# Performance work log

Hardware: AMD Instinct MI355X
Metric: run time of the kernel (lower is better)

## Reference

```python
import jax, jax.numpy as jnp
import numpy as np

N, R, M, E, NE, B = 50000, 500, 120000, 960000, 800000, 8192
D, H1, HID, OC = 200, 256, 512, 50


def setup_inputs() -> dict:
    key = jax.random.key(0)
    ks = jax.random.split(key, 26)
    s = 0.05
    rn = lambda k, shp: jax.random.normal(k, shp, jnp.float32) * s
    return {
        "entity_emb": jax.random.normal(ks[0], (N, D), jnp.float32),
        "rel_emb": jax.random.normal(ks[1], (R, D), jnp.float32),
        "b_x": jax.random.randint(ks[2], (M,), 0, N),
        "b_node_graph_index": jax.random.randint(ks[3], (M,), 0, R),
        "edge_src": jax.random.randint(ks[4], (E,), 0, M),
        "edge_dst": jax.random.randint(ks[5], (E,), 0, M),
        "edge_w": jax.random.uniform(ks[6], (E,), jnp.float32),
        "big_src": jax.random.randint(ks[7], (NE,), 0, N),
        "big_dst": jax.random.randint(ks[8], (NE,), 0, N),
        "big_w": jax.random.uniform(ks[9], (NE,), jnp.float32),
        "perm": jax.random.permutation(ks[10], N),
        "batch_inputs": jnp.stack([
            jax.random.randint(ks[11], (B,), 0, N),
            jax.random.randint(ks[12], (B,), 0, R),
            jax.random.randint(ks[13], (B,), 0, N)], axis=1),
        "W1a": rn(ks[14], (2 * D, H1)), "W1b": rn(ks[15], (H1, D)),
        "W2a": rn(ks[16], (D, H1)), "W2b": rn(ks[17], (H1, D)),
        "Wle": rn(ks[18], (2 * D, 1)), "ble": jnp.zeros((1,), jnp.float32),
        "Wlo": rn(ks[19], (2 * D, D)), "blo": jnp.zeros((D,), jnp.float32),
        "Wg": rn(ks[20], (D, HID)), "Wd": rn(ks[21], (HID, HID)),
        "conv_w": rn(ks[22], (OC, 3)), "conv_b": jnp.zeros((OC,), jnp.float32),
        "fc_w": rn(ks[23], (OC * D, 1)), "fc_b": jnp.zeros((1,), jnp.float32),
    }


def _l2norm(x):
    return x / jnp.maximum(jnp.linalg.norm(x, axis=-1, keepdims=True), 1e-12)


def _gcn(x, src, dst, w, n, Wa, Wb):
    # two-layer GCN over sparse edge list: out = A @ relu(A @ x @ Wa) @ Wb
    agg = lambda h: jax.ops.segment_sum(h[src] * w[:, None], dst, num_segments=n)
    h = jax.nn.relu(agg(x) @ Wa)
    return agg(h) @ Wb


def _seg_softmax(v, idx, n):
    m = jax.ops.segment_max(v, idx, num_segments=n)
    e = jnp.exp(v - m[idx])
    s = jax.ops.segment_sum(e, idx, num_segments=n)
    return e / (s[idx] + 1e-16)


def _mce(ent, rel, b_x, b_gi, src, dst, w, W1a, W1b, Wle, ble, Wlo, blo):
    x = jnp.concatenate([ent[b_x], rel[b_gi]], axis=-1)          # [M, 400]
    e = _gcn(x, src, dst, w, b_x.shape[0], W1a, W1b)             # [M, 200]
    cnt = jax.ops.segment_sum(jnp.ones((b_x.shape[0],), e.dtype), b_x, num_segments=N)
    mean = jax.ops.segment_sum(e, b_x, num_segments=N) / jnp.maximum(cnt, 1.0)[:, None]
    z = mean[b_x]                                                # scatter_mean then gather
    emb = jnp.concatenate([e[b_x], z], axis=-1)                  # [M, 400]
    score = emb @ Wle + ble                                      # [M, 1]
    zs = _seg_softmax(score, b_x, N)                             # segment softmax
    pooled = jax.ops.segment_sum(zs * emb, b_x, num_segments=N)  # [N, 400]
    return (pooled @ Wlo + blo) + ent


def _dgi(h1, h2, Wg, Wd):
    p1 = jax.nn.relu(h1 @ Wg)
    p2 = jax.nn.relu(h2 @ Wg)
    c = jax.nn.sigmoid(jnp.mean(p1, axis=0))                     # readout [HID]
    t = Wd @ c
    return jnp.concatenate([p1 @ t, p2 @ t])                     # [2N]


def _convkb(trip, conv_w, conv_b, fc_w, fc_b):
    # trip [B,3,D]; Conv2d(1, OC, (1,3)) over [B,1,D,3] -> [B,OC,D]
    h = jax.nn.relu(jnp.einsum('bsd,os->bod', trip, conv_w) + conv_b[None, :, None])
    return h.reshape(trip.shape[0], -1) @ fc_w + fc_b            # [B,1]


def reference(entity_emb, rel_emb, b_x, b_node_graph_index, edge_src, edge_dst,
              edge_w, big_src, big_dst, big_w, perm, batch_inputs,
              W1a, W1b, W2a, W2b, Wle, ble, Wlo, blo, Wg, Wd,
              conv_w, conv_b, fc_w, fc_b):
    ent = _l2norm(entity_emb)
    rel = _l2norm(rel_emb)
    ent_shuf = ent[perm]
    ec = _mce(ent, rel, b_x, b_node_graph_index, edge_src, edge_dst, edge_w,
              W1a, W1b, Wle, ble, Wlo, blo)
    ec_ = _mce(ent_shuf, rel, b_x, b_node_graph_index, edge_src, edge_dst, edge_w,
               W1a, W1b, Wle, ble, Wlo, blo)
    eg = _gcn(ec, big_src, big_dst, big_w, N, W2a, W2b)
    eg_ = _gcn(ec_, big_src, big_dst, big_w, N, W2a, W2b)
    local_logits = _dgi(ec, ec_, Wg, Wd)
    global_logits = _dgi(eg, eg_, Wg, Wd)
    trip = jnp.stack([ec[batch_inputs[:, 0]], rel[batch_inputs[:, 1]],
                      ec[batch_inputs[:, 2]]], axis=1)           # [B,3,D]
    out_conv = _convkb(trip, conv_w, conv_b, fc_w, fc_b)
    return out_conv, local_logits, global_logits
```

## Files before the change

kernel.cpp:

```cpp
#include <hip/hip_runtime.h>

#define NN   50000
#define RR   500
#define MM   120000
#define EE   960000
#define NEE  800000
#define BB   8192
#define DD   200
#define HH1  256
#define HIDD 512
#define OCC  50

typedef unsigned int  u32;
typedef unsigned short u16;
typedef __attribute__((ext_vector_type(8))) short bf16x8;
typedef __attribute__((ext_vector_type(4))) float f32x4;

static __device__ __forceinline__ float bf2f(u16 u) {
    u32 x = ((u32)u) << 16;
    return __uint_as_float(x);
}
static __device__ __forceinline__ u16 f2bf(float f) {
    u32 x = __float_as_uint(f);
    u32 r = (x + 0x7FFFu + ((x >> 16) & 1u)) >> 16;
    return (u16)r;
}
static __device__ __forceinline__ u32 pack2(float a, float b) {
    return (u32)f2bf(a) | ((u32)f2bf(b) << 16);
}
static __device__ __forceinline__ void unpack2(u32 v, float& a, float& b) {
    a = bf2f((u16)(v & 0xFFFFu));
    b = bf2f((u16)(v >> 16));
}

static __device__ __forceinline__ float wredsum(float v) {
#pragma unroll
    for (int off = 32; off > 0; off >>= 1) v += __shfl_xor(v, off);
    return v;
}

static __device__ __forceinline__ u32 relu2bf(u32 x) {
    if (x & 0x00008000u) x &= 0xFFFF0000u;
    if (x & 0x80000000u) x &= 0x0000FFFFu;
    return x;
}
static __device__ __forceinline__ bf16x8 zero8() {
    bf16x8 z;
#pragma unroll
    for (int i = 0; i < 8; ++i) z[i] = 0;
    return z;
}

__global__ void k_l2norm(const float* __restrict__ in, float* __restrict__ outf,
                         u16* __restrict__ outb, int rows) {
    int w = (blockIdx.x * blockDim.x + threadIdx.x) >> 6;
    int lane = threadIdx.x & 63;
    if (w >= rows) return;
    const float* r = in + (size_t)w * DD;
    float s = 0.f;
    for (int d = lane; d < DD; d += 64) { float v = r[d]; s += v * v; }
    s = wredsum(s);
    float inv = 1.0f / fmaxf(sqrtf(s), 1e-12f);
    for (int d = lane; d < DD; d += 64) {
        float v = r[d] * inv;
        if (outf) outf[(size_t)w * DD + d] = v;
        if (outb) outb[(size_t)w * DD + d] = f2bf(v);
    }
}

__global__ void k_gather_perm(const int* __restrict__ bx, const int* __restrict__ perm,
                              int* __restrict__ idx1, int M) {
    int m = blockIdx.x * blockDim.x + threadIdx.x;
    if (m < M) idx1[m] = perm[bx[m]];
}

__global__ void k_edge_idx(const int* __restrict__ srcE, const int* __restrict__ map,
                           int* __restrict__ outE, int n) {
    int e = blockIdx.x * blockDim.x + threadIdx.x;
    if (e < n) outE[e] = map[srcE[e]];
}

__global__ void k_prepw(const float* __restrict__ src, int Nc, int Kd,
                        u16* __restrict__ hi, u16* __restrict__ lo) {
    int i = blockIdx.x * blockDim.x + threadIdx.x;
    if (i >= Nc * Kd) return;
    int n = i / Kd, k = i - n * Kd;
    float b = src[(size_t)k * Nc + n];
    u16 hb_ = f2bf(b);
    hi[i] = hb_;
    lo[i] = f2bf(b - bf2f(hb_));
}

__global__ void k_hist(const int* __restrict__ idx, int* __restrict__ cnt, int n) {
    int i = blockIdx.x * blockDim.x + threadIdx.x;
    if (i < n) atomicAdd(&cnt[idx[i]], 1);
}

__global__ __launch_bounds__(1024) void k_scan(const int* __restrict__ in,
                                               int* __restrict__ out, int n) {
    __shared__ int wtot[16];
    __shared__ int wexc[16];
    __shared__ int s_carry;
    int tid = threadIdx.x, lane = tid & 63, wid = tid >> 6;
    if (tid == 0) s_carry = 0;
    __syncthreads();
    for (int base = 0; base < n; base += 1024) {
        int i = base + tid;
        int v = (i < n) ? in[i] : 0;
        int x = v;
#pragma unroll
        for (int off = 1; off < 64; off <<= 1) {
            int t = __shfl_up(x, off);
            if (lane >= off) x += t;
        }
        if (lane == 63) wtot[wid] = x;
        __syncthreads();
        if (wid == 0) {
            int wv2 = (lane < 16) ? wtot[lane] : 0;
            int y = wv2;
#pragma unroll
            for (int off = 1; off < 16; off <<= 1) {
                int t = __shfl_up(y, off);
                if (lane >= off) y += t;
            }
            if (lane < 16) wexc[lane] = y - wv2;
            if (lane == 15) wtot[15] = y;
        }
        __syncthreads();
        if (i < n) out[i] = s_carry + wexc[wid] + (x - v);
        int chunk_total = wtot[15];
        __syncthreads();
        if (tid == 0) s_carry += chunk_total;
        __syncthreads();
    }
    if (threadIdx.x == 0) out[n] = s_carry;
}

__global__ void k_fill2(const int* __restrict__ dst, const int* __restrict__ src,
                        const float* __restrict__ w, int* __restrict__ cursor,
                        int* __restrict__ srcs_out, float* __restrict__ ws_out, int n) {
    int e = blockIdx.x * blockDim.x + threadIdx.x;
    if (e >= n) return;
    int p = atomicAdd(&cursor[dst[e]], 1);
    srcs_out[p] = src[e];
    ws_out[p] = w[e];
}

__global__ void k_fill1(const int* __restrict__ idx, int* __restrict__ cursor,
                        int* __restrict__ outm, int n) {
    int m = blockIdx.x * blockDim.x + threadIdx.x;
    if (m >= n) return;
    int p = atomicAdd(&cursor[idx[m]], 1);
    outm[p] = m;
}

__global__ void k_pull_mce(const int* __restrict__ rp, const int* __restrict__ ivE,
                           const int* __restrict__ giE, const float* __restrict__ wE,
                           const u16* __restrict__ Pent, const u16* __restrict__ Prel,
                           u16* __restrict__ out, int ndst) {
    int wv = (blockIdx.x * blockDim.x + threadIdx.x) >> 6;
    if (wv >= ndst) return;
    int lane = threadIdx.x & 63;
    int beg = rp[wv], end = rp[wv + 1];
    float accA[2] = {0.f, 0.f}, accB[2] = {0.f, 0.f};
    int e = beg;
    for (; e + 4 <= end; e += 4) {
        int i0 = ivE[e], i1 = ivE[e + 1], i2 = ivE[e + 2], i3 = ivE[e + 3];
        int g0 = giE[e], g1 = giE[e + 1], g2 = giE[e + 2], g3 = giE[e + 3];
        float w0 = wE[e], w1 = wE[e + 1], w2 = wE[e + 2], w3 = wE[e + 3];
        const u32* pe0 = (const u32*)(Pent + (size_t)i0 * HH1);
        const u32* pe1 = (const u32*)(Pent + (size_t)i1 * HH1);
        const u32* pe2 = (const u32*)(Pent + (size_t)i2 * HH1);
        const u32* pe3 = (const u32*)(Pent + (size_t)i3 * HH1);
        const u32* pr0 = (const u32*)(Prel + (size_t)g0 * HH1);
        const u32* pr1 = (const u32*)(Prel + (size_t)g1 * HH1);
        const u32* pr2 = (const u32*)(Prel + (size_t)g2 * HH1);
        const u32* pr3 = (const u32*)(Prel + (size_t)g3 * HH1);
        u32 vp[4][2], vr[4][2];
#pragma unroll
        for (int t = 0; t < 2; ++t) {
            int p = lane + 64 * t;
            vp[0][t] = pe0[p]; vp[1][t] = pe1[p]; vp[2][t] = pe2[p]; vp[3][t] = pe3[p];
            vr[0][t] = pr0[p]; vr[1][t] = pr1[p]; vr[2][t] = pr2[p]; vr[3][t] = pr3[p];
        }
#pragma unroll
        for (int t = 0; t < 2; ++t) {
            float a, b, c, d;
            unpack2(vp[0][t], a, b); unpack2(vr[0][t], c, d);
            accA[t] += (a + c) * w0; accB[t] += (b + d) * w0;
            unpack2(vp[1][t], a, b); unpack2(vr[1][t], c, d);
            accA[t] += (a + c) * w1; accB[t] += (b + d) * w1;
            unpack2(vp[2][t], a, b); unpack2(vr[2][t], c, d);
            accA[t] += (a + c) * w2; accB[t] += (b + d) * w2;
            unpack2(vp[3][t], a, b); unpack2(vr[3][t], c, d);
            accA[t] += (a + c) * w3; accB[t] += (b + d) * w3;
        }
    }
    for (; e < end; ++e) {
        int iv = ivE[e], gi = giE[e];
        float w = wE[e];
        const u32* pe = (const u32*)(Pent + (size_t)iv * HH1);
        const u32* pr = (const u32*)(Prel + (size_t)gi * HH1);
#pragma unroll
        for (int t = 0; t < 2; ++t) {
            int p = lane + 64 * t;
            float a, b, c, d;
            unpack2(pe[p], a, b); unpack2(pr[p], c, d);
            accA[t] += (a + c) * w; accB[t] += (b + d) * w;
        }
    }
    u32* o = (u32*)(out + (size_t)wv * HH1);
#pragma unroll
    for (int t = 0; t < 2; ++t) o[lane + 64 * t] = pack2(accA[t], accB[t]);
}

template<int DIMS, int INS, int OUTS>
__global__ void k_pull(const int* __restrict__ rp, const int* __restrict__ srcs,
                       const float* __restrict__ wsrt,
                       const u16* __restrict__ inh, const u16* __restrict__ inl,
                       u16* __restrict__ outh, u16* __restrict__ outl, int ndst) {
    int wv = (blockIdx.x * blockDim.x + threadIdx.x) >> 6;
    if (wv >= ndst) return;
    int lane = threadIdx.x & 63;
    int beg = rp[wv], end = rp[wv + 1];
    constexpr int NP = DIMS / 2;
    constexpr int NT = (NP + 63) / 64;
    float accA[NT], accB[NT];
#pragma unroll
    for (int t = 0; t < NT; ++t) { accA[t] = 0.f; accB[t] = 0.f; }
    int e = beg;
    for (; e + 4 <= end; e += 4) {
        int s0 = srcs[e], s1 = srcs[e + 1], s2 = srcs[e + 2], s3 = srcs[e + 3];
        float w0 = wsrt[e], w1 = wsrt[e + 1], w2 = wsrt[e + 2], w3 = wsrt[e + 3];
        const u32* rh[4] = {
            (const u32*)(inh + (size_t)s0 * DIMS), (const u32*)(inh + (size_t)s1 * DIMS),
            (const u32*)(inh + (size_t)s2 * DIMS), (const u32*)(inh + (size_t)s3 * DIMS)};
        u32 vh[4][NT], vl[4][NT];
#pragma unroll
        for (int t = 0; t < NT; ++t) {
            int p = lane + 64 * t;
            if (p < NP) {
                vh[0][t] = rh[0][p]; vh[1][t] = rh[1][p];
                vh[2][t] = rh[2][p]; vh[3][t] = rh[3][p];
            }
        }
        if (INS) {
            const u32* rl[4] = {
                (const u32*)(inl + (size_t)s0 * DIMS), (const u32*)(inl + (size_t)s1 * DIMS),
                (const u32*)(inl + (size_t)s2 * DIMS), (const u32*)(inl + (size_t)s3 * DIMS)};
#pragma unroll
            for (int t = 0; t < NT; ++t) {
                int p = lane + 64 * t;
                if (p < NP) {
                    vl[0][t] = rl[0][p]; vl[1][t] = rl[1][p];
                    vl[2][t] = rl[2][p]; vl[3][t] = rl[3][p];
                }
            }
        }
        float ws[4] = {w0, w1, w2, w3};
#pragma unroll
        for (int q = 0; q < 4; ++q) {
#pragma unroll
            for (int t = 0; t < NT; ++t) {
                int p = lane + 64 * t;
                if (p < NP) {
                    float a, b;
                    unpack2(vh[q][t], a, b);
                    if (INS) { float a2, b2; unpack2(vl[q][t], a2, b2); a += a2; b += b2; }
                    accA[t] += a * ws[q]; accB[t] += b * ws[q];
                }
            }
        }
    }
    for (; e < end; ++e) {
        int s = srcs[e];
        float w = wsrt[e];
        const u32* rh = (const u32*)(inh + (size_t)s * DIMS);
        const u32* rl = INS ? (const u32*)(inl + (size_t)s * DIMS) : nullptr;
#pragma unroll
        for (int t = 0; t < NT; ++t) {
            int p = lane + 64 * t;
            if (p < NP) {
                float a, b;
                unpack2(rh[p], a, b);
                if (INS) { float a2, b2; unpack2(rl[p], a2, b2); a += a2; b += b2; }
                accA[t] += a * w; accB[t] += b * w;
            }
        }
    }
    u32* oh = (u32*)(outh + (size_t)wv * DIMS);
    u32* ol = OUTS ? (u32*)(outl + (size_t)wv * DIMS) : nullptr;
#pragma unroll
    for (int t = 0; t < NT; ++t) {
        int p = lane + 64 * t;
        if (p < NP) {
            if (OUTS == 0) {
                oh[p] = pack2(accA[t], accB[t]);
            } else {
                u16 ha = f2bf(accA[t]), hb_ = f2bf(accB[t]);
                u16 la = f2bf(accA[t] - bf2f(ha)), lb = f2bf(accB[t] - bf2f(hb_));
                oh[p] = (u32)ha | ((u32)hb_ << 16);
                ol[p] = (u32)la | ((u32)lb << 16);
            }
        }
    }
}

__global__ void k_segpool(const int* __restrict__ rpX, const int* __restrict__ mids,
                          const u16* __restrict__ e_buf, u16* __restrict__ pooled, int n) {
    int nv = (blockIdx.x * blockDim.x + threadIdx.x) >> 6;
    if (nv >= n) return;
    int lane = threadIdx.x & 63;
    int beg = rpX[nv], end = rpX[nv + 1];
    int cnt = end - beg;
    float accA[2] = {0.f, 0.f}, accB[2] = {0.f, 0.f};
    int e = beg;
    for (; e + 4 <= end; e += 4) {
        const u32* r0 = (const u32*)(e_buf + (size_t)mids[e] * DD);
        const u32* r1 = (const u32*)(e_buf + (size_t)mids[e + 1] * DD);
        const u32* r2 = (const u32*)(e_buf + (size_t)mids[e + 2] * DD);
        const u32* r3 = (const u32*)(e_buf + (size_t)mids[e + 3] * DD);
        u32 v[4][2];
#pragma unroll
        for (int t = 0; t < 2; ++t) {
            int p = lane + 64 * t;
            if (p < DD / 2) { v[0][t] = r0[p]; v[1][t] = r1[p]; v[2][t] = r2[p]; v[3][t] = r3[p]; }
        }
#pragma unroll
        for (int t = 0; t < 2; ++t) {
            int p = lane + 64 * t;
            if (p < DD / 2) {
                float a, b;
                unpack2(v[0][t], a, b); accA[t] += a; accB[t] += b;
                unpack2(v[1][t], a, b); accA[t] += a; accB[t] += b;
                unpack2(v[2][t], a, b); accA[t] += a; accB[t] += b;
                unpack2(v[3][t], a, b); accA[t] += a; accB[t] += b;
            }
        }
    }
    for (; e < end; ++e) {
        const u32* r = (const u32*)(e_buf + (size_t)mids[e] * DD);
#pragma unroll
        for (int t = 0; t < 2; ++t) {
            int p = lane + 64 * t;
            if (p < DD / 2) { float a, b; unpack2(r[p], a, b); accA[t] += a; accB[t] += b; }
        }
    }
    float inv = 1.0f / fmaxf((float)cnt, 1.0f);
    bool occ = cnt > 0;
    const u32* er = (const u32*)(e_buf + (size_t)nv * DD);
    u32* p0 = (u32*)(pooled + (size_t)nv * (2 * DD));
#pragma unroll
    for (int t = 0; t < 2; ++t) {
        int p = lane + 64 * t;
        if (p < DD / 2) {
            p0[p] = occ ? er[p] : 0u;
            p0[DD / 2 + p] = occ ? pack2(accA[t] * inv, accB[t] * inv) : 0u;
        }
    }
}

template<int AMODE, int RELU_IN, int RELU_OUT, int HAS_BIAS, int HAS_ADD, int FUSE, int CMODE>
__global__ __launch_bounds__(256, 2) void k_mfmamm(
    const u16* __restrict__ Ah, const u16* __restrict__ Al,
    const u16* __restrict__ Bh, const u16* __restrict__ Bl,
    void* __restrict__ Cv, u16* __restrict__ Cl,
    int Mr, int Nc, int Kd,
    const float* __restrict__ bias, const u16* __restrict__ addsrc,
    const int* __restrict__ addidx, const float* __restrict__ tvec,
    float* __restrict__ redout) {
    constexpr int BM = 128, BN = 128, BK = 32;
    constexpr int ASTR = 40;
    __shared__ u16 Ahs[BM * ASTR];
    __shared__ u16 Als[AMODE ? (BM * ASTR) : 8];

    int tid = threadIdx.x;
    int wid = tid >> 6, lane = tid & 63;
    int wr = wid >> 1, wc = wid & 1;
    int r = lane & 15, h = lane >> 4;
    int bm0 = blockIdx.y * BM, bn0 = blockIdx.x * BN;
    int srow = (tid & 15) + 16 * (tid >> 6);
    int sg = (tid >> 4) & 3;

    f32x4 acc[4][4];
#pragma unroll
    for (int i = 0; i < 4; ++i)
#pragma unroll
        for (int j = 0; j < 4; ++j) acc[i][j] = (f32x4){0.f, 0.f, 0.f, 0.f};

    for (int k0 = 0; k0 < Kd; k0 += BK) {
        __syncthreads();
        int kc = k0 + sg * 8;
        bool kok = (kc + 8 <= Kd);
#pragma unroll
        for (int it = 0; it < 2; ++it) {
            int row = srow + 64 * it;
            int gr = bm0 + row;
            uint4 v = make_uint4(0, 0, 0, 0), vl = make_uint4(0, 0, 0, 0);
            if (gr < Mr && kok) {
                v = *(const uint4*)(Ah + (size_t)gr * Kd + kc);
                if (AMODE) vl = *(const uint4*)(Al + (size_t)gr * Kd + kc);
            }
            if (RELU_IN) {
                v.x = relu2bf(v.x); v.y = relu2bf(v.y);
                v.z = relu2bf(v.z); v.w = relu2bf(v.w);
            }
            *(uint4*)(Ahs + row * ASTR + sg * 8) = v;
            if (AMODE) *(uint4*)(Als + row * ASTR + sg * 8) = vl;
        }
        __syncthreads();
        bf16x8 bh[4], bl[4];
        int kb = k0 + h * 8;
        bool kbok = (kb + 8 <= Kd);
#pragma unroll
        for (int j = 0; j < 4; ++j) {
            int nrow = bn0 + wc * 64 + j * 16 + r;
            if (nrow < Nc && kbok) {
                bh[j] = *(const bf16x8*)(Bh + (size_t)nrow * Kd + kb);
                bl[j] = *(const bf16x8*)(Bl + (size_t)nrow * Kd + kb);
            } else { bh[j] = zero8(); bl[j] = zero8(); }
        }
        bf16x8 af[4], al[4];
#pragma unroll
        for (int i = 0; i < 4; ++i) {
            int mrow = wr * 64 + i * 16 + r;
            af[i] = *(const bf16x8*)(Ahs + mrow * ASTR + h * 8);
            if (AMODE) al[i] = *(const bf16x8*)(Als + mrow * ASTR + h * 8);
        }
#pragma unroll
        for (int i = 0; i < 4; ++i)
#pragma unroll
            for (int j = 0; j < 4; ++j) {
                acc[i][j] = __builtin_amdgcn_mfma_f32_16x16x32_bf16(af[i], bh[j], acc[i][j], 0, 0, 0);
                acc[i][j] = __builtin_amdgcn_mfma_f32_16x16x32_bf16(af[i], bl[j], acc[i][j], 0, 0, 0);
                if (AMODE)
                    acc[i][j] = __builtin_amdgcn_mfma_f32_16x16x32_bf16(al[i], bh[j], acc[i][j], 0, 0, 0);
            }
    }
    float colacc[4] = {0.f, 0.f, 0.f, 0.f};
#pragma unroll
    for (int i = 0; i < 4; ++i) {
        float rowacc[4] = {0.f, 0.f, 0.f, 0.f};
#pragma unroll
        for (int j = 0; j < 4; ++j) {
            int col = bn0 + wc * 64 + j * 16 + r;
            bool colok = col < Nc;
            float tv = (FUSE == 2 && colok) ? tvec[col] : 0.f;
#pragma unroll
            for (int rg = 0; rg < 4; ++rg) {
                int row = bm0 + wr * 64 + i * 16 + h * 4 + rg;
                float v = acc[i][j][rg];
                if (HAS_BIAS && colok) v += bias[col];
                if (RELU_OUT) v = fmaxf(v, 0.f);
                bool ok = colok && row < Mr;
                if (HAS_ADD && ok) {
                    int r2 = addidx ? addidx[row] : row;
                    v += bf2f(addsrc[(size_t)r2 * Nc + col]);
                }
                if (FUSE != 2 && ok) {
                    size_t cidx = (size_t)row * Nc + col;
                    if (CMODE == 0) ((u16*)Cv)[cidx] = f2bf(v);
                    else if (CMODE == 1) ((float*)Cv)[cidx] = v;
                    else {
                        u16 hi_ = f2bf(v);
                        ((u16*)Cv)[cidx] = hi_;
                        Cl[cidx] = f2bf(v - bf2f(hi_));
                    }
                }
                if (FUSE == 1 && ok) colacc[j] += v;
                if (FUSE == 2) rowacc[rg] += v * tv;
            }
        }
        if (FUSE == 2) {
#pragma unroll
            for (int rg = 0; rg < 4; ++rg) {
                float val = rowacc[rg];
                val += __shfl_xor(val, 1); val += __shfl_xor(val, 2);
                val += __shfl_xor(val, 4); val += __shfl_xor(val, 8);
                int row = bm0 + wr * 64 + i * 16 + h * 4 + rg;
                if (r == 0 && row < Mr) atomicAdd(&redout[row], val);
            }
        }
    }
    if (FUSE == 1) {
#pragma unroll
        for (int j = 0; j < 4; ++j) {
            float val = colacc[j];
            val += __shfl_xor(val, 16); val += __shfl_xor(val, 32);
            int col = bn0 + wc * 64 + j * 16 + r;
            if (h == 0 && col < Nc) atomicAdd(&redout[col], val);
        }
    }
}

__global__ void k_sigc(const float* __restrict__ csum, float* __restrict__ cvec) {
    int i = threadIdx.x;
    cvec[i] = 1.0f / (1.0f + expf(-csum[i] * (1.0f / (float)NN)));
}

__global__ void k_tmv(const float* __restrict__ Wd, const float* __restrict__ cvec,
                      float* __restrict__ tvec) {
    __shared__ float c[HIDD];
    int lane = threadIdx.x;
    for (int j = lane; j < HIDD; j += 64) c[j] = cvec[j];
    __syncthreads();
    int r0 = blockIdx.x * 16;
    for (int i = r0; i < r0 + 16; ++i) {
        const float* wr = Wd + (size_t)i * HIDD;
        float s = 0.f;
        for (int j = lane; j < HIDD; j += 64) s += wr[j] * c[j];
        s = wredsum(s);
        if (lane == 0) tvec[i] = s;
    }
}

__global__ void k_rowdot512(const float* __restrict__ p, const float* __restrict__ t,
                            float* __restrict__ out, int rows) {
    int g = blockIdx.x * blockDim.x + threadIdx.x;
    int wv = g >> 6;
    if (wv >= rows) return;
    int lane = g & 63;
    const float* r = p + (size_t)wv * HIDD;
    float s = 0.f;
#pragma unroll
    for (int t4 = 0; t4 < 8; ++t4) {
        int d = lane + t4 * 64;
        s += r[d] * t[d];
    }
    s = wredsum(s);
    if (lane == 0) out[wv] = s;
}

__global__ void k_convkb(const u16* __restrict__ ec, const float* __restrict__ rel,
                         const int* __restrict__ bi, const float* __restrict__ cw,
                         const float* __restrict__ cb, const float* __restrict__ fcw,
                         const float* __restrict__ fcb, float* __restrict__ out) {
    __shared__ float t0[DD], t1[DD], t2[DD];
    __shared__ float red[4];
    int b = blockIdx.x, tid = threadIdx.x;
    int i0 = bi[b * 3 + 0], i1 = bi[b * 3 + 1], i2 = bi[b * 3 + 2];
    if (tid < DD) {
        t0[tid] = bf2f(ec[(size_t)i0 * DD + tid]);
        t1[tid] = rel[(size_t)i1 * DD + tid];
        t2[tid] = bf2f(ec[(size_t)i2 * DD + tid]);
    }
    __syncthreads();
    float partial = 0.f;
    if (tid < DD) {
        float a = t0[tid], bb = t1[tid], c = t2[tid];
        for (int o = 0; o < OCC; ++o) {
            float h = fmaxf(cw[o * 3 + 0] * a + cw[o * 3 + 1] * bb + cw[o * 3 + 2] * c + cb[o], 0.f);
            partial += h * fcw[o * DD + tid];
        }
    }
    partial = wredsum(partial);
    if ((tid & 63) == 0) red[tid >> 6] = partial;
    __syncthreads();
    if (tid == 0) out[b] = red[0] + red[1] + red[2] + red[3] + fcb[0];
}

__global__ void k_sentinel(float* out, float val) { out[threadIdx.x] = val; }

extern "C" void kernel_launch(void* const* d_in, const int* in_sizes, int n_in,
                              void* d_out, int out_size, void* d_ws, size_t ws_size,
                              hipStream_t stream) {
    const float* entity_emb = (const float*)d_in[0];
    const float* rel_emb    = (const float*)d_in[1];
    const int*   b_x        = (const int*)d_in[2];
    const int*   b_gi       = (const int*)d_in[3];
    const int*   e_src      = (const int*)d_in[4];
    const int*   e_dst      = (const int*)d_in[5];
    const float* e_w        = (const float*)d_in[6];
    const int*   big_src    = (const int*)d_in[7];
    const int*   big_dst    = (const int*)d_in[8];
    const float* big_w      = (const float*)d_in[9];
    const int*   perm       = (const int*)d_in[10];
    const int*   batch_in   = (const int*)d_in[11];
    const float* W1a        = (const float*)d_in[12];
    const float* W1b        = (const float*)d_in[13];
    const float* W2a        = (const float*)d_in[14];
    const float* W2b        = (const float*)d_in[15];
    const float* Wlo        = (const float*)d_in[18];
    const float* blo        = (const float*)d_in[19];
    const float* Wg         = (const float*)d_in[20];
    const float* Wd         = (const float*)d_in[21];
    const float* conv_w     = (const float*)d_in[22];
    const float* conv_b     = (const float*)d_in[23];
    const float* fc_w       = (const float*)d_in[24];
    const float* fc_b       = (const float*)d_in[25];
    float* out = (float*)d_out;

    size_t off = 0;
    auto balloc = [&](size_t nbytes) {
        size_t p = off;
        off += (nbytes + 511) & ~(size_t)511;
        return p;
    };
    char* base = (char*)d_ws;
    u16*   entb = (u16*)(base + balloc((size_t)NN * DD * 2));
    float* relf = (float*)(base + balloc((size_t)RR * DD * 4));
    u16*   relb = (u16*)(base + balloc((size_t)RR * DD * 2));
    u16*   Pent = (u16*)(base + balloc((size_t)NN * HH1 * 2));
    u16*   Prel = (u16*)(base + balloc((size_t)RR * HH1 * 2));
    int*   idx1 = (int*)(base + balloc((size_t)MM * 4));
    u16*   ecb  = (u16*)(base + balloc((size_t)NN * DD * 2));
    int*   rpB  = (int*)(base + balloc((size_t)(NN + 1) * 4));
    int*   srcB = (int*)(base + balloc((size_t)NEE * 4));
    float* wB   = (float*)(base + balloc((size_t)NEE * 4));
    int*   rpE  = (int*)(base + balloc((size_t)(MM + 1) * 4));
    int*   srcE = (int*)(base + balloc((size_t)EE * 4));
    float* wE   = (float*)(base + balloc((size_t)EE * 4));
    int*   ivE  = (int*)(base + balloc((size_t)EE * 4));
    int*   giE  = (int*)(base + balloc((size_t)EE * 4));
    int*   rpX  = (int*)(base + balloc((size_t)(NN + 1) * 4));
    int*   mids = (int*)(base + balloc((size_t)MM * 4));
    int*   curB = (int*)(base + balloc((size_t)NN * 4));
    int*   curE = (int*)(base + balloc((size_t)MM * 4));
    int*   curX = (int*)(base + balloc((size_t)NN * 4));
    u16* w1aT_h  = (u16*)(base + balloc(200 * 256 * 2));
    u16* w1aT_l  = (u16*)(base + balloc(200 * 256 * 2));
    u16* w1abT_h = (u16*)(base + balloc(200 * 256 * 2));
    u16* w1abT_l = (u16*)(base + balloc(200 * 256 * 2));
    u16* w1bT_h  = (u16*)(base + balloc(256 * 200 * 2));
    u16* w1bT_l  = (u16*)(base + balloc(256 * 200 * 2));
    u16* wloT_h  = (u16*)(base + balloc(400 * 200 * 2));
    u16* wloT_l  = (u16*)(base + balloc(400 * 200 * 2));
    u16* wgT_h   = (u16*)(base + balloc(200 * 512 * 2));
    u16* wgT_l   = (u16*)(base + balloc(200 * 512 * 2));
    u16* w2aT_h  = (u16*)(base + balloc(200 * 256 * 2));
    u16* w2aT_l  = (u16*)(base + balloc(200 * 256 * 2));
    u16* w2bT_h  = (u16*)(base + balloc(256 * 200 * 2));
    u16* w2bT_l  = (u16*)(base + balloc(256 * 200 * 2));
    char*  Aarena = base + balloc((size_t)MM * HH1 * 2);
    char*  Barena = base + balloc((size_t)MM * DD * 2);
    char*  Carena = base + balloc((size_t)MM * DD * 2);
    float* csum = (float*)(base + balloc(4 * 2048));
    float* cvec = csum + 512;
    float* t_l  = csum + 1024;
    float* t_g  = csum + 1536;

    if (ws_size < off) {
        k_sentinel<<<dim3(1), dim3(8), 0, stream>>>(out, (float)(ws_size >> 20));
        return;
    }

    const size_t PL = 20000000;
    u16*   aggx   = (u16*)Aarena;
    u16*   hb     = (u16*)Barena;
    u16*   e_buf  = (u16*)Carena;
    u16*   pooled = (u16*)Aarena;
    u16*   a1h    = (u16*)Aarena;
    u16*   a1l    = (u16*)(Aarena + PL);
    u16*   h2h    = (u16*)Barena;
    u16*   h2l    = (u16*)(Barena + 25600000);
    u16*   h2bh   = (u16*)Aarena;
    u16*   h2bl   = (u16*)(Aarena + PL);
    u16*   egh    = (u16*)Carena;
    u16*   egl    = (u16*)(Carena + PL);
    float* pbuf   = (float*)Aarena;

    dim3 blk(256);
    auto wgrid = [](int items) { return dim3((unsigned)((items + 3) / 4)); };
    auto tgrid = [](int items) { return dim3((unsigned)((items + 255) / 256)); };
    auto mmgrid = [](int Mr, int Nc) { return dim3((unsigned)((Nc + 127) / 128), (unsigned)((Mr + 127) / 128)); };

    k_l2norm<<<wgrid(NN), blk, 0, stream>>>(entity_emb, nullptr, entb, NN);
    k_l2norm<<<wgrid(RR), blk, 0, stream>>>(rel_emb, relf, relb, RR);
    k_gather_perm<<<tgrid(MM), blk, 0, stream>>>(b_x, perm, idx1, MM);
    k_prepw<<<tgrid(256 * 200), blk, 0, stream>>>(W1a, 256, 200, w1aT_h, w1aT_l);
    k_prepw<<<tgrid(256 * 200), blk, 0, stream>>>(W1a + 200 * 256, 256, 200, w1abT_h, w1abT_l);
    k_prepw<<<tgrid(200 * 256), blk, 0, stream>>>(W1b, 200, 256, w1bT_h, w1bT_l);
    k_prepw<<<tgrid(200 * 400), blk, 0, stream>>>(Wlo, 200, 400, wloT_h, wloT_l);
    k_prepw<<<tgrid(512 * 200), blk, 0, stream>>>(Wg, 512, 200, wgT_h, wgT_l);
    k_prepw<<<tgrid(256 * 200), blk, 0, stream>>>(W2a, 256, 200, w2aT_h, w2aT_l);
    k_prepw<<<tgrid(200 * 256), blk, 0, stream>>>(W2b, 200, 256, w2bT_h, w2bT_l);

    hipMemsetAsync(curB, 0, (size_t)NN * 4, stream);
    hipMemsetAsync(curE, 0, (size_t)MM * 4, stream);
    hipMemsetAsync(curX, 0, (size_t)NN * 4, stream);
    k_hist<<<tgrid(NEE), blk, 0, stream>>>(big_dst, curB, NEE);
    k_hist<<<tgrid(EE), blk, 0, stream>>>(e_dst, curE, EE);
    k_hist<<<tgrid(MM), blk, 0, stream>>>(b_x, curX, MM);
    k_scan<<<dim3(1), dim3(1024), 0, stream>>>(curB, rpB, NN);
    k_scan<<<dim3(1), dim3(1024), 0, stream>>>(curE, rpE, MM);
    k_scan<<<dim3(1), dim3(1024), 0, stream>>>(curX, rpX, NN);
    hipMemcpyAsync(curB, rpB, (size_t)NN * 4, hipMemcpyDeviceToDevice, stream);
    hipMemcpyAsync(curE, rpE, (size_t)MM * 4, hipMemcpyDeviceToDevice, stream);
    hipMemcpyAsync(curX, rpX, (size_t)NN * 4, hipMemcpyDeviceToDevice, stream);
    k_fill2<<<tgrid(NEE), blk, 0, stream>>>(big_dst, big_src, big_w, curB, srcB, wB, NEE);
    k_fill2<<<tgrid(EE), blk, 0, stream>>>(e_dst, e_src, e_w, curE, srcE, wE, EE);
    k_fill1<<<tgrid(MM), blk, 0, stream>>>(b_x, curX, mids, MM);
    k_edge_idx<<<tgrid(EE), blk, 0, stream>>>(srcE, b_gi, giE, EE);

    k_mfmamm<0, 0, 0, 0, 0, 0, 0><<<mmgrid(NN, HH1), blk, 0, stream>>>(
        entb, nullptr, w1aT_h, w1aT_l, Pent, nullptr, NN, HH1, DD,
        nullptr, nullptr, nullptr, nullptr, nullptr);
    k_mfmamm<0, 0, 0, 0, 0, 0, 0><<<mmgrid(RR, HH1), blk, 0, stream>>>(
        relb, nullptr, w1abT_h, w1abT_l, Prel, nullptr, RR, HH1, DD,
        nullptr, nullptr, nullptr, nullptr, nullptr);

    for (int v = 0; v < 2; ++v) {
        const int* ivmap  = v ? idx1 : b_x;
        const int* addidx = v ? perm : nullptr;

        k_edge_idx<<<tgrid(EE), blk, 0, stream>>>(srcE, ivmap, ivE, EE);
        k_pull_mce<<<wgrid(MM), blk, 0, stream>>>(rpE, ivE, giE, wE, Pent, Prel, aggx, MM);
        k_mfmamm<0, 1, 0, 0, 0, 0, 0><<<mmgrid(MM, DD), blk, 0, stream>>>(
            aggx, nullptr, w1bT_h, w1bT_l, hb, nullptr, MM, DD, HH1,
            nullptr, nullptr, nullptr, nullptr, nullptr);
        k_pull<DD, 0, 0><<<wgrid(MM), blk, 0, stream>>>(rpE, srcE, wE, hb, nullptr,
                                                        e_buf, nullptr, MM);
        k_segpool<<<wgrid(NN), blk, 0, stream>>>(rpX, mids, e_buf, pooled, NN);
        k_mfmamm<0, 0, 0, 1, 1, 0, 0><<<mmgrid(NN, DD), blk, 0, stream>>>(
            pooled, nullptr, wloT_h, wloT_l, ecb, nullptr, NN, DD, 2 * DD,
            blo, entb, addidx, nullptr, nullptr);

        if (v == 0) {
            hipMemsetAsync(csum, 0, 512 * sizeof(float), stream);
            k_mfmamm<0, 0, 1, 0, 0, 1, 1><<<mmgrid(NN, HIDD), blk, 0, stream>>>(
                ecb, nullptr, wgT_h, wgT_l, pbuf, nullptr, NN, HIDD, DD,
                nullptr, nullptr, nullptr, nullptr, csum);
            k_sigc<<<dim3(1), dim3(512), 0, stream>>>(csum, cvec);
            k_tmv<<<dim3(32), dim3(64), 0, stream>>>(Wd, cvec, t_l);
            k_rowdot512<<<wgrid(NN), blk, 0, stream>>>(pbuf, t_l, out + BB, NN);
            k_convkb<<<dim3(BB), blk, 0, stream>>>(ecb, relf, batch_in,
                                                   conv_w, conv_b, fc_w, fc_b, out);
        } else {
            hipMemsetAsync(out + BB + NN, 0, (size_t)NN * 4, stream);
            k_mfmamm<0, 0, 1, 0, 0, 2, 1><<<mmgrid(NN, HIDD), blk, 0, stream>>>(
                ecb, nullptr, wgT_h, wgT_l, nullptr, nullptr, NN, HIDD, DD,
                nullptr, nullptr, nullptr, t_l, out + BB + NN);
        }

        k_pull<DD, 0, 1><<<wgrid(NN), blk, 0, stream>>>(rpB, srcB, wB, ecb, nullptr,
                                                        a1h, a1l, NN);
        k_mfmamm<1, 0, 1, 0, 0, 0, 2><<<mmgrid(NN, HH1), blk, 0, stream>>>(
            a1h, a1l, w2aT_h, w2aT_l, h2h, h2l, NN, HH1, DD,
            nullptr, nullptr, nullptr, nullptr, nullptr);
        k_mfmamm<1, 0, 0, 0, 0, 0, 2><<<mmgrid(NN, DD), blk, 0, stream>>>(
            h2h, h2l, w2bT_h, w2bT_l, h2bh, h2bl, NN, DD, HH1,
            nullptr, nullptr, nullptr, nullptr, nullptr);
        k_pull<DD, 1, 1><<<wgrid(NN), blk, 0, stream>>>(rpB, srcB, wB, h2bh, h2bl,
                                                        egh, egl, NN);

        if (v == 0) {
            hipMemsetAsync(csum, 0, 512 * sizeof(float), stream);
            k_mfmamm<1, 0, 1, 0, 0, 1, 1><<<mmgrid(NN, HIDD), blk, 0, stream>>>(
                egh, egl, wgT_h, wgT_l, pbuf, nullptr, NN, HIDD, DD,
                nullptr, nullptr, nullptr, nullptr, csum);
            k_sigc<<<dim3(1), dim3(512), 0, stream>>>(csum, cvec);
            k_tmv<<<dim3(32), dim3(64), 0, stream>>>(Wd, cvec, t_g);
            k_rowdot512<<<wgrid(NN), blk, 0, stream>>>(pbuf, t_g, out + BB + 2 * (size_t)NN, NN);
        } else {
            hipMemsetAsync(out + BB + 3 * (size_t)NN, 0, (size_t)NN * 4, stream);
            k_mfmamm<1, 0, 1, 0, 0, 2, 1><<<mmgrid(NN, HIDD), blk, 0, stream>>>(
                egh, egl, wgT_h, wgT_l, nullptr, nullptr, NN, HIDD, DD,
                nullptr, nullptr, nullptr, t_g, out + BB + 3 * (size_t)NN);
        }
    }

    (void)in_sizes; (void)n_in; (void)out_size;
}
```

Before: 2.324 ms.

## Double-buffer A tiles in shared memory for MFMA GEMM with register prefetch

The MFMA GEMM kernel now keeps two shared-memory buffers for the A tile. The next K-slice is prefetched from global memory into registers while the current slice is computed, then written into the alternate buffer. This cuts one barrier per iteration and hides global load latency behind the MFMA work. In exchange it uses more shared memory and registers, and the launch bounds no longer request 2 blocks per CU, which may reduce occupancy.

```diff
diff --git a/kernel.cpp b/kernel.cpp
--- a/kernel.cpp
+++ b/kernel.cpp
@@ -361,7 +361,7 @@
 }
 
 template<int AMODE, int RELU_IN, int RELU_OUT, int HAS_BIAS, int HAS_ADD, int FUSE, int CMODE>
-__global__ __launch_bounds__(256, 2) void k_mfmamm(
+__global__ __launch_bounds__(256) void k_mfmamm(
     const u16* __restrict__ Ah, const u16* __restrict__ Al,
     const u16* __restrict__ Bh, const u16* __restrict__ Bl,
     void* __restrict__ Cv, u16* __restrict__ Cl,
@@ -371,8 +371,8 @@
     float* __restrict__ redout) {
     constexpr int BM = 128, BN = 128, BK = 32;
     constexpr int ASTR = 40;
-    __shared__ u16 Ahs[BM * ASTR];
-    __shared__ u16 Als[AMODE ? (BM * ASTR) : 8];
+    __shared__ u16 Ahs[2][BM * ASTR];
+    __shared__ u16 Als[AMODE ? 2 : 1][AMODE ? (BM * ASTR) : 8];
 
     int tid = threadIdx.x;
     int wid = tid >> 6, lane = tid & 63;
@@ -381,6 +381,7 @@
     int bm0 = blockIdx.y * BM, bn0 = blockIdx.x * BN;
     int srow = (tid & 15) + 16 * (tid >> 6);
     int sg = (tid >> 4) & 3;
+    int nk = (Kd + BK - 1) / BK;
 
     f32x4 acc[4][4];
 #pragma unroll
@@ -388,54 +389,97 @@
 #pragma unroll
         for (int j = 0; j < 4; ++j) acc[i][j] = (f32x4){0.f, 0.f, 0.f, 0.f};
 
-    for (int k0 = 0; k0 < Kd; k0 += BK) {
-        __syncthreads();
-        int kc = k0 + sg * 8;
+    uint4 pa[2], pl[2];
+    {
+        int kc = sg * 8;
         bool kok = (kc + 8 <= Kd);
 #pragma unroll
         for (int it = 0; it < 2; ++it) {
             int row = srow + 64 * it;
             int gr = bm0 + row;
-            uint4 v = make_uint4(0, 0, 0, 0), vl = make_uint4(0, 0, 0, 0);
+            uint4 v = make_uint4(0, 0, 0, 0), vl2 = make_uint4(0, 0, 0, 0);
             if (gr < Mr && kok) {
                 v = *(const uint4*)(Ah + (size_t)gr * Kd + kc);
-                if (AMODE) vl = *(const uint4*)(Al + (size_t)gr * Kd + kc);
+                if (AMODE) vl2 = *(const uint4*)(Al + (size_t)gr * Kd + kc);
             }
             if (RELU_IN) {
                 v.x = relu2bf(v.x); v.y = relu2bf(v.y);
                 v.z = relu2bf(v.z); v.w = relu2bf(v.w);
             }
-            *(uint4*)(Ahs + row * ASTR + sg * 8) = v;
-            if (AMODE) *(uint4*)(Als + row * ASTR + sg * 8) = vl;
-        }
-        __syncthreads();
-        bf16x8 bh[4], bl[4];
-        int kb = k0 + h * 8;
-        bool kbok = (kb + 8 <= Kd);
-#pragma unroll
-        for (int j = 0; j < 4; ++j) {
-            int nrow = bn0 + wc * 64 + j * 16 + r;
-            if (nrow < Nc && kbok) {
-                bh[j] = *(const bf16x8*)(Bh + (size_t)nrow * Kd + kb);
-                bl[j] = *(const bf16x8*)(Bl + (size_t)nrow * Kd + kb);
-            } else { bh[j] = zero8(); bl[j] = zero8(); }
-        }
-        bf16x8 af[4], al[4];
+            pa[it] = v;
+            if (AMODE) pl[it] = vl2;
+        }
+#pragma unroll
+        for (int it = 0; it < 2; ++it) {
+            int row = srow + 64 * it;
+            *(uint4*)(&Ahs[0][row * ASTR + sg * 8]) = pa[it];
+            if (AMODE) *(uint4*)(&Als[0][row * ASTR + sg * 8]) = pl[it];
+        }
+    }
+    __syncthreads();
+
+    for (int k = 0; k < nk; ++k) {
+        int cur = k & 1;
+        uint4 na[2], nl[2];
+        bool have_next = (k + 1 < nk);
+        if (have_next) {
+            int kc = (k + 1) * BK + sg * 8;
+            bool kok = (kc + 8 <= Kd);
+#pragma unroll
+            for (int it = 0; it < 2; ++it) {
+                int row = srow + 64 * it;
+                int gr = bm0 + row;
+                uint4 v = make_uint4(0, 0, 0, 0), vl2 = make_uint4(0, 0, 0, 0);
+                if (gr < Mr && kok) {
+                    v = *(const uint4*)(Ah + (size_t)gr * Kd + kc);
+                    if (AMODE) vl2 = *(const uint4*)(Al + (size_t)gr * Kd + kc);
+                }
+                if (RELU_IN) {
+                    v.x = relu2bf(v.x); v.y = relu2bf(v.y);
+                    v.z = relu2bf(v.z); v.w = relu2bf(v.w);
+                }
+                na[it] = v;
+                if (AMODE) nl[it] = vl2;
+            }
+        }
+        bf16x8 bh4[4], bl4[4];
+        {
+            int kb = k * BK + h * 8;
+            bool kbok = (kb + 8 <= Kd);
+#pragma unroll
+            for (int j = 0; j < 4; ++j) {
+                int nrow = bn0 + wc * 64 + j * 16 + r;
+                if (nrow < Nc && kbok) {
+                    bh4[j] = *(const bf16x8*)(Bh + (size_t)nrow * Kd + kb);
+                    bl4[j] = *(const bf16x8*)(Bl + (size_t)nrow * Kd + kb);
+                } else { bh4[j] = zero8(); bl4[j] = zero8(); }
+            }
+        }
+        bf16x8 af[4], alr[4];
 #pragma unroll
         for (int i = 0; i < 4; ++i) {
             int mrow = wr * 64 + i * 16 + r;
-            af[i] = *(const bf16x8*)(Ahs + mrow * ASTR + h * 8);
-            if (AMODE) al[i] = *(const bf16x8*)(Als + mrow * ASTR + h * 8);
+            af[i] = *(const bf16x8*)(&Ahs[cur][mrow * ASTR + h * 8]);
+            if (AMODE) alr[i] = *(const bf16x8*)(&Als[cur][mrow * ASTR + h * 8]);
         }
 #pragma unroll
         for (int i = 0; i < 4; ++i)
 #pragma unroll
             for (int j = 0; j < 4; ++j) {
-                acc[i][j] = __builtin_amdgcn_mfma_f32_16x16x32_bf16(af[i], bh[j], acc[i][j], 0, 0, 0);
-                acc[i][j] = __builtin_amdgcn_mfma_f32_16x16x32_bf16(af[i], bl[j], acc[i][j], 0, 0, 0);
+                acc[i][j] = __builtin_amdgcn_mfma_f32_16x16x32_bf16(af[i], bh4[j], acc[i][j], 0, 0, 0);
+                acc[i][j] = __builtin_amdgcn_mfma_f32_16x16x32_bf16(af[i], bl4[j], acc[i][j], 0, 0, 0);
                 if (AMODE)
-                    acc[i][j] = __builtin_amdgcn_mfma_f32_16x16x32_bf16(al[i], bh[j], acc[i][j], 0, 0, 0);
-            }
+                    acc[i][j] = __builtin_amdgcn_mfma_f32_16x16x32_bf16(alr[i], bh4[j], acc[i][j], 0, 0, 0);
+            }
+        if (have_next) {
+#pragma unroll
+            for (int it = 0; it < 2; ++it) {
+                int row = srow + 64 * it;
+                *(uint4*)(&Ahs[cur ^ 1][row * ASTR + sg * 8]) = na[it];
+                if (AMODE) *(uint4*)(&Als[cur ^ 1][row * ASTR + sg * 8]) = nl[it];
+            }
+        }
+        __syncthreads();
     }
     float colacc[4] = {0.f, 0.f, 0.f, 0.f};
 #pragma unroll
```

New measurement: 2.250 ms. 3.2% less time.

## Drop LDS staging in MFMA GEMM, load A directly with compile-time K

Applied to the files above, without the earlier changes.

The GEMM kernel stops staging the A tile through shared memory with two barriers per K-step. Each wave now loads its A and B fragments straight from global memory into registers. K becomes a template parameter so the K loop fully unrolls, and launch_bounds drops the min-blocks-per-CU hint. This removes LDS traffic and synchronisation, but A rows are no longer shared between the two column waves, so global/L2 reads roughly double and register pressure rises.

```diff
diff --git a/kernel.cpp b/kernel.cpp
--- a/kernel.cpp
+++ b/kernel.cpp
@@ -49,6 +49,12 @@
 #pragma unroll
     for (int i = 0; i < 8; ++i) z[i] = 0;
     return z;
+}
+static __device__ __forceinline__ bf16x8 relu8(bf16x8 v) {
+    uint4 u = *(uint4*)&v;
+    u.x = relu2bf(u.x); u.y = relu2bf(u.y);
+    u.z = relu2bf(u.z); u.w = relu2bf(u.w);
+    return *(bf16x8*)&u;
 }
 
 __global__ void k_l2norm(const float* __restrict__ in, float* __restrict__ outf,
@@ -360,27 +366,40 @@
     }
 }
 
-template<int AMODE, int RELU_IN, int RELU_OUT, int HAS_BIAS, int HAS_ADD, int FUSE, int CMODE>
-__global__ __launch_bounds__(256, 2) void k_mfmamm(
+template<int KD, int AMODE, int RELU_IN, int RELU_OUT, int HAS_BIAS, int HAS_ADD, int FUSE, int CMODE>
+__global__ __launch_bounds__(256) void k_mfmamm(
     const u16* __restrict__ Ah, const u16* __restrict__ Al,
     const u16* __restrict__ Bh, const u16* __restrict__ Bl,
     void* __restrict__ Cv, u16* __restrict__ Cl,
-    int Mr, int Nc, int Kd,
+    int Mr, int Nc,
     const float* __restrict__ bias, const u16* __restrict__ addsrc,
     const int* __restrict__ addidx, const float* __restrict__ tvec,
     float* __restrict__ redout) {
-    constexpr int BM = 128, BN = 128, BK = 32;
-    constexpr int ASTR = 40;
-    __shared__ u16 Ahs[BM * ASTR];
-    __shared__ u16 Als[AMODE ? (BM * ASTR) : 8];
-
+    constexpr int NK = (KD + 31) / 32;
     int tid = threadIdx.x;
     int wid = tid >> 6, lane = tid & 63;
     int wr = wid >> 1, wc = wid & 1;
     int r = lane & 15, h = lane >> 4;
-    int bm0 = blockIdx.y * BM, bn0 = blockIdx.x * BN;
-    int srow = (tid & 15) + 16 * (tid >> 6);
-    int sg = (tid >> 4) & 3;
+    int bm0 = blockIdx.y * 128, bn0 = blockIdx.x * 128;
+
+    const u16* arow[4];
+    const u16* lrow[4];
+#pragma unroll
+    for (int i = 0; i < 4; ++i) {
+        int grow = bm0 + wr * 64 + i * 16 + r;
+        if (grow >= Mr) grow = Mr - 1;
+        arow[i] = Ah + (size_t)grow * KD;
+        if (AMODE) lrow[i] = Al + (size_t)grow * KD;
+    }
+    const u16* brow[4];
+    const u16* blrow[4];
+#pragma unroll
+    for (int j = 0; j < 4; ++j) {
+        int nrow = bn0 + wc * 64 + j * 16 + r;
+        int nc = (nrow < Nc) ? nrow : 0;
+        brow[j] = Bh + (size_t)nc * KD;
+        blrow[j] = Bl + (size_t)nc * KD;
+    }
 
     f32x4 acc[4][4];
 #pragma unroll
@@ -388,53 +407,30 @@
 #pragma unroll
         for (int j = 0; j < 4; ++j) acc[i][j] = (f32x4){0.f, 0.f, 0.f, 0.f};
 
-    for (int k0 = 0; k0 < Kd; k0 += BK) {
-        __syncthreads();
-        int kc = k0 + sg * 8;
-        bool kok = (kc + 8 <= Kd);
-#pragma unroll
-        for (int it = 0; it < 2; ++it) {
-            int row = srow + 64 * it;
-            int gr = bm0 + row;
-            uint4 v = make_uint4(0, 0, 0, 0), vl = make_uint4(0, 0, 0, 0);
-            if (gr < Mr && kok) {
-                v = *(const uint4*)(Ah + (size_t)gr * Kd + kc);
-                if (AMODE) vl = *(const uint4*)(Al + (size_t)gr * Kd + kc);
-            }
-            if (RELU_IN) {
-                v.x = relu2bf(v.x); v.y = relu2bf(v.y);
-                v.z = relu2bf(v.z); v.w = relu2bf(v.w);
-            }
-            *(uint4*)(Ahs + row * ASTR + sg * 8) = v;
-            if (AMODE) *(uint4*)(Als + row * ASTR + sg * 8) = vl;
-        }
-        __syncthreads();
-        bf16x8 bh[4], bl[4];
-        int kb = k0 + h * 8;
-        bool kbok = (kb + 8 <= Kd);
+#pragma unroll
+    for (int k = 0; k < NK; ++k) {
+        int kb = k * 32 + h * 8;
+        bool kok = (kb + 8 <= KD);
+        bf16x8 a4[4], al4[4], b4[4], bl4[4];
 #pragma unroll
         for (int j = 0; j < 4; ++j) {
-            int nrow = bn0 + wc * 64 + j * 16 + r;
-            if (nrow < Nc && kbok) {
-                bh[j] = *(const bf16x8*)(Bh + (size_t)nrow * Kd + kb);
-                bl[j] = *(const bf16x8*)(Bl + (size_t)nrow * Kd + kb);
-            } else { bh[j] = zero8(); bl[j] = zero8(); }
-        }
-        bf16x8 af[4], al[4];
+            b4[j] = kok ? *(const bf16x8*)(brow[j] + kb) : zero8();
+            bl4[j] = kok ? *(const bf16x8*)(blrow[j] + kb) : zero8();
+        }
 #pragma unroll
         for (int i = 0; i < 4; ++i) {
-            int mrow = wr * 64 + i * 16 + r;
-            af[i] = *(const bf16x8*)(Ahs + mrow * ASTR + h * 8);
-            if (AMODE) al[i] = *(const bf16x8*)(Als + mrow * ASTR + h * 8);
+            a4[i] = kok ? *(const bf16x8*)(arow[i] + kb) : zero8();
+            if (RELU_IN) a4[i] = relu8(a4[i]);
+            if (AMODE) al4[i] = kok ? *(const bf16x8*)(lrow[i] + kb) : zero8();
         }
 #pragma unroll
         for (int i = 0; i < 4; ++i)
 #pragma unroll
             for (int j = 0; j < 4; ++j) {
-                acc[i][j] = __builtin_amdgcn_mfma_f32_16x16x32_bf16(af[i], bh[j], acc[i][j], 0, 0, 0);
-                acc[i][j] = __builtin_amdgcn_mfma_f32_16x16x32_bf16(af[i], bl[j], acc[i][j], 0, 0, 0);
+                acc[i][j] = __builtin_amdgcn_mfma_f32_16x16x32_bf16(a4[i], b4[j], acc[i][j], 0, 0, 0);
+                acc[i][j] = __builtin_amdgcn_mfma_f32_16x16x32_bf16(a4[i], bl4[j], acc[i][j], 0, 0, 0);
                 if (AMODE)
-                    acc[i][j] = __builtin_amdgcn_mfma_f32_16x16x32_bf16(al[i], bh[j], acc[i][j], 0, 0, 0);
+                    acc[i][j] = __builtin_amdgcn_mfma_f32_16x16x32_bf16(al4[i], b4[j], acc[i][j], 0, 0, 0);
             }
     }
     float colacc[4] = {0.f, 0.f, 0.f, 0.f};
@@ -692,11 +688,11 @@
     k_fill1<<<tgrid(MM), blk, 0, stream>>>(b_x, curX, mids, MM);
     k_edge_idx<<<tgrid(EE), blk, 0, stream>>>(srcE, b_gi, giE, EE);
 
-    k_mfmamm<0, 0, 0, 0, 0, 0, 0><<<mmgrid(NN, HH1), blk, 0, stream>>>(
-        entb, nullptr, w1aT_h, w1aT_l, Pent, nullptr, NN, HH1, DD,
+    k_mfmamm<200, 0, 0, 0, 0, 0, 0, 0><<<mmgrid(NN, HH1), blk, 0, stream>>>(
+        entb, nullptr, w1aT_h, w1aT_l, Pent, nullptr, NN, HH1,
         nullptr, nullptr, nullptr, nullptr, nullptr);
-    k_mfmamm<0, 0, 0, 0, 0, 0, 0><<<mmgrid(RR, HH1), blk, 0, stream>>>(
-        relb, nullptr, w1abT_h, w1abT_l, Prel, nullptr, RR, HH1, DD,
+    k_mfmamm<200, 0, 0, 0, 0, 0, 0, 0><<<mmgrid(RR, HH1), blk, 0, stream>>>(
+        relb, nullptr, w1abT_h, w1abT_l, Prel, nullptr, RR, HH1,
         nullptr, nullptr, nullptr, nullptr, nullptr);
 
     for (int v = 0; v < 2; ++v) {
@@ -705,20 +701,20 @@
 
         k_edge_idx<<<tgrid(EE), blk, 0, stream>>>(srcE, ivmap, ivE, EE);
         k_pull_mce<<<wgrid(MM), blk, 0, stream>>>(rpE, ivE, giE, wE, Pent, Prel, aggx, MM);
-        k_mfmamm<0, 1, 0, 0, 0, 0, 0><<<mmgrid(MM, DD), blk, 0, stream>>>(
-            aggx, nullptr, w1bT_h, w1bT_l, hb, nullptr, MM, DD, HH1,
+        k_mfmamm<256, 0, 1, 0, 0, 0, 0, 0><<<mmgrid(MM, DD), blk, 0, stream>>>(
+            aggx, nullptr, w1bT_h, w1bT_l, hb, nullptr, MM, DD,
             nullptr, nullptr, nullptr, nullptr, nullptr);
         k_pull<DD, 0, 0><<<wgrid(MM), blk, 0, stream>>>(rpE, srcE, wE, hb, nullptr,
                                                         e_buf, nullptr, MM);
         k_segpool<<<wgrid(NN), blk, 0, stream>>>(rpX, mids, e_buf, pooled, NN);
-        k_mfmamm<0, 0, 0, 1, 1, 0, 0><<<mmgrid(NN, DD), blk, 0, stream>>>(
-            pooled, nullptr, wloT_h, wloT_l, ecb, nullptr, NN, DD, 2 * DD,
+        k_mfmamm<400, 0, 0, 0, 1, 1, 0, 0><<<mmgrid(NN, DD), blk, 0, stream>>>(
+            pooled, nullptr, wloT_h, wloT_l, ecb, nullptr, NN, DD,
             blo, entb, addidx, nullptr, nullptr);
 
         if (v == 0) {
             hipMemsetAsync(csum, 0, 512 * sizeof(float), stream);
-            k_mfmamm<0, 0, 1, 0, 0, 1, 1><<<mmgrid(NN, HIDD), blk, 0, stream>>>(
-                ecb, nullptr, wgT_h, wgT_l, pbuf, nullptr, NN, HIDD, DD,
+            k_mfmamm<200, 0, 0, 1, 0, 0, 1, 1><<<mmgrid(NN, HIDD), blk, 0, stream>>>(
+                ecb, nullptr, wgT_h, wgT_l, pbuf, nullptr, NN, HIDD,
                 nullptr, nullptr, nullptr, nullptr, csum);
             k_sigc<<<dim3(1), dim3(512), 0, stream>>>(csum, cvec);
             k_tmv<<<dim3(32), dim3(64), 0, stream>>>(Wd, cvec, t_l);
@@ -727,34 +723,34 @@
                                                    conv_w, conv_b, fc_w, fc_b, out);
         } else {
             hipMemsetAsync(out + BB + NN, 0, (size_t)NN * 4, stream);
-            k_mfmamm<0, 0, 1, 0, 0, 2, 1><<<mmgrid(NN, HIDD), blk, 0, stream>>>(
-                ecb, nullptr, wgT_h, wgT_l, nullptr, nullptr, NN, HIDD, DD,
+            k_mfmamm<200, 0, 0, 1, 0, 0, 2, 1><<<mmgrid(NN, HIDD), blk, 0, stream>>>(
+                ecb, nullptr, wgT_h, wgT_l, nullptr, nullptr, NN, HIDD,
                 nullptr, nullptr, nullptr, t_l, out + BB + NN);
         }
 
         k_pull<DD, 0, 1><<<wgrid(NN), blk, 0, stream>>>(rpB, srcB, wB, ecb, nullptr,
                                                         a1h, a1l, NN);
-        k_mfmamm<1, 0, 1, 0, 0, 0, 2><<<mmgrid(NN, HH1), blk, 0, stream>>>(
-            a1h, a1l, w2aT_h, w2aT_l, h2h, h2l, NN, HH1, DD,
+        k_mfmamm<200, 1, 0, 1, 0, 0, 0, 2><<<mmgrid(NN, HH1), blk, 0, stream>>>(
+            a1h, a1l, w2aT_h, w2aT_l, h2h, h2l, NN, HH1,
             nullptr, nullptr, nullptr, nullptr, nullptr);
-        k_mfmamm<1, 0, 0, 0, 0, 0, 2><<<mmgrid(NN, DD), blk, 0, stream>>>(
-            h2h, h2l, w2bT_h, w2bT_l, h2bh, h2bl, NN, DD, HH1,
+        k_mfmamm<256, 1, 0, 0, 0, 0, 0, 2><<<mmgrid(NN, DD), blk, 0, stream>>>(
+            h2h, h2l, w2bT_h, w2bT_l, h2bh, h2bl, NN, DD,
             nullptr, nullptr, nullptr, nullptr, nullptr);
         k_pull<DD, 1, 1><<<wgrid(NN), blk, 0, stream>>>(rpB, srcB, wB, h2bh, h2bl,
                                                         egh, egl, NN);
 
         if (v == 0) {
             hipMemsetAsync(csum, 0, 512 * sizeof(float), stream);
-            k_mfmamm<1, 0, 1, 0, 0, 1, 1><<<mmgrid(NN, HIDD), blk, 0, stream>>>(
-                egh, egl, wgT_h, wgT_l, pbuf, nullptr, NN, HIDD, DD,
+            k_mfmamm<200, 1, 0, 1, 0, 0, 1, 1><<<mmgrid(NN, HIDD), blk, 0, stream>>>(
+                egh, egl, wgT_h, wgT_l, pbuf, nullptr, NN, HIDD,
                 nullptr, nullptr, nullptr, nullptr, csum);
             k_sigc<<<dim3(1), dim3(512), 0, stream>>>(csum, cvec);
             k_tmv<<<dim3(32), dim3(64), 0, stream>>>(Wd, cvec, t_g);
             k_rowdot512<<<wgrid(NN), blk, 0, stream>>>(pbuf, t_g, out + BB + 2 * (size_t)NN, NN);
         } else {
             hipMemsetAsync(out + BB + 3 * (size_t)NN, 0, (size_t)NN * 4, stream);
-            k_mfmamm<1, 0, 1, 0, 0, 2, 1><<<mmgrid(NN, HIDD), blk, 0, stream>>>(
-                egh, egl, wgT_h, wgT_l, nullptr, nullptr, NN, HIDD, DD,
+            k_mfmamm<200, 1, 0, 1, 0, 0, 2, 1><<<mmgrid(NN, HIDD), blk, 0, stream>>>(
+                egh, egl, wgT_h, wgT_l, nullptr, nullptr, NN, HIDD,
                 nullptr, nullptr, nullptr, t_g, out + BB + 3 * (size_t)NN);
         }
     }
```

After: 2.388 ms. 1.03x slower.
